# Kernel tuning notes

Hardware: AMD Instinct MI355X
Metric: run time of the kernel (lower is better)

## Reference

```python
import jax, jax.numpy as jnp
import numpy as np

HIDDEN = 1024
B, S = 64, 512
EPS = 1e-10


def setup_inputs() -> dict:
    key = jax.random.key(0)
    k1, k2, k3, k4, k5 = jax.random.split(key, 5)
    encoder_outputs = jax.random.normal(k1, (B, S, HIDDEN), dtype=jnp.float32)
    decoder_hidden = jax.random.normal(k2, (B, HIDDEN), dtype=jnp.float32)
    inp_mask = (jax.random.uniform(k3, (S, B)) > 0.2).astype(jnp.float32)
    # W_h: Linear(2H -> H, bias=False); torch stores weight as (out, in)
    W_h = jax.random.normal(k4, (HIDDEN, 2 * HIDDEN), dtype=jnp.float32) / np.sqrt(2 * HIDDEN)
    stdv = 1.0 / np.sqrt(HIDDEN)
    v = jax.random.normal(k5, (HIDDEN,), dtype=jnp.float32) * stdv
    return {"encoder_outputs": encoder_outputs, "decoder_hidden": decoder_hidden,
            "inp_mask": inp_mask, "W_h": W_h, "v": v}


def reference(encoder_outputs, decoder_hidden, inp_mask, W_h, v):
    # encoder_outputs: [B, S, H]; decoder_hidden: [B, H]; inp_mask: [S, B]
    seq_len = encoder_outputs.shape[1]
    # H = decoder_hidden broadcast over seq: [B, S, H] (avoid explicit repeat)
    Hrep = jnp.broadcast_to(decoder_hidden[:, None, :], encoder_outputs.shape)
    cat = jnp.concatenate([Hrep, encoder_outputs], axis=2)          # [B, S, 2H]
    energy = jnp.tanh(jnp.einsum('bsk,hk->bsh', cat, W_h))          # [B, S, H]
    scores = jnp.einsum('bsh,h->bs', energy, v)                     # [B, S]
    # NOTE: original applies softmax over dim=0 (the batch dim) — faithful here
    a = jax.nn.softmax(scores, axis=0) * inp_mask.T                 # [B, S]
    a = a / (jnp.sum(a, axis=1, keepdims=True) + EPS)
    context = jnp.einsum('bs,bsh->bh', a, encoder_outputs)[:, None, :]  # [B, 1, H]
    return a[:, None, :], context
```

## Files before the change

### kernel.cpp

```cpp
#include <hip/hip_runtime.h>

#define B_ 64
#define S_ 512
#define H_ 1024
#define M_ (B_*S_)

typedef unsigned int u32;
typedef unsigned short u16;
typedef __attribute__((ext_vector_type(8))) short bf16x8;
typedef __attribute__((ext_vector_type(4))) float f32x4;

__device__ __forceinline__ u16 f2bf(float f) {
  u32 u = __builtin_bit_cast(u32, f);
  u += 0x7fffu + ((u >> 16) & 1u);
  return (u16)(u >> 16);
}
__device__ __forceinline__ u32 pk2(float a, float b) {
  return (u32)f2bf(a) | ((u32)f2bf(b) << 16);
}
__device__ __forceinline__ float tanh_fast(float x) {
  x = fminf(fmaxf(x, -20.f), 20.f);
  float e = __expf(2.f * x);
  return (e - 1.f) / (e + 1.f);
}
__device__ __forceinline__ void gload_lds16(const u16* g, u16* l) {
  __builtin_amdgcn_global_load_lds(
      (const __attribute__((address_space(1))) u32*)g,
      (__attribute__((address_space(3))) u32*)l, 16, 0, 0);
}

__global__ void conv_w2(const float* __restrict__ Wh, u16* __restrict__ W2bf) {
  int idx = blockIdx.x * 256 + threadIdx.x;
  int n = idx >> 8;
  int k = (idx & 255) * 4;
  float4 x = *(const float4*)(Wh + (size_t)n * 2048 + 1024 + k);
  uint2 p; p.x = pk2(x.x, x.y); p.y = pk2(x.z, x.w);
  *(uint2*)(W2bf + (size_t)n * 1024 + k) = p;
}

__global__ void part1_kernel(const float* __restrict__ dh,
                             const float* __restrict__ Wh,
                             float* __restrict__ part1) {
  __shared__ float whs[16][132];
  __shared__ float dhs[64][132];
  int t = threadIdx.x;
  int h0 = blockIdx.x * 16;
  int k0 = blockIdx.y * 128;
#pragma unroll
  for (int i = 0; i < 2; ++i) {
    int idx = t + 256 * i;
    int r = idx >> 5, c4 = idx & 31;
    float4 x = *(const float4*)(Wh + (size_t)(h0 + r) * 2048 + k0 + c4 * 4);
    *(float4*)&whs[r][c4 * 4] = x;
  }
#pragma unroll
  for (int i = 0; i < 8; ++i) {
    int idx = t + 256 * i;
    int r = idx >> 5, c4 = idx & 31;
    float4 x = *(const float4*)(dh + (size_t)r * 1024 + k0 + c4 * 4);
    *(float4*)&dhs[r][c4 * 4] = x;
  }
  __syncthreads();
  int b = t >> 2, hg = t & 3;
  float acc[4] = {0.f, 0.f, 0.f, 0.f};
#pragma unroll 4
  for (int k = 0; k < 128; ++k) {
    float d = dhs[b][k];
#pragma unroll
    for (int j = 0; j < 4; ++j) acc[j] += whs[hg * 4 + j][k] * d;
  }
#pragma unroll
  for (int j = 0; j < 4; ++j)
    atomicAdd(&part1[b * 1024 + h0 + hg * 4 + j], acc[j]);
}

__global__ __launch_bounds__(256, 2) void gemm_scores(
    const float* __restrict__ enc, const u16* __restrict__ W2bf,
    const float* __restrict__ part1, const float* __restrict__ v,
    float* __restrict__ scores) {
  __shared__ __align__(16) u16 As[2][128 * 64];
  __shared__ __align__(16) u16 Bs[2][128 * 64];
  __shared__ float sc_lds[128];
  const int tid = threadIdx.x;
  const int lane = tid & 63, wid = tid >> 6;
  const int wr = wid >> 1, wc = wid & 1;
  const int l15 = lane & 15, lhi = lane >> 4;
  const int n0 = blockIdx.x * 128;
  const int r0 = blockIdx.y * 128;
  const int bb = r0 >> 9;

  f32x4 acc[4][4] = {};

  const int brow8 = lane >> 3;
  const int bks = ((lane & 7) ^ brow8) * 8;

  {
#pragma unroll
    for (int c = 0; c < 4; ++c) {
      const u16* src = W2bf + (size_t)(n0 + c * 32 + wid * 8 + brow8) * 1024 + bks;
      gload_lds16(src, &Bs[0][c * 2048 + wid * 512]);
    }
#pragma unroll
    for (int i = 0; i < 4; ++i) {
      int f = 2 * tid + 512 * i;
      int arow = f >> 4, c4 = f & 15;
      const float4* srcA = (const float4*)(enc + (size_t)(r0 + arow) * 1024 + c4 * 4);
      float4 x = srcA[0], y = srcA[1];
      uint4 p; p.x = pk2(x.x, x.y); p.y = pk2(x.z, x.w);
      p.z = pk2(y.x, y.y); p.w = pk2(y.z, y.w);
      *(uint4*)&As[0][arow * 64 + ((c4 * 4) ^ ((arow & 7) << 3))] = p;
    }
    __syncthreads();
  }

  int p = 0;
  for (int t = 0; t < 16; ++t) {
    float4 xa[4], ya[4];
    if (t < 15) {
      const int kn = (t + 1) * 64;
#pragma unroll
      for (int c = 0; c < 4; ++c) {
        const u16* src =
            W2bf + (size_t)(n0 + c * 32 + wid * 8 + brow8) * 1024 + kn + bks;
        gload_lds16(src, &Bs[p ^ 1][c * 2048 + wid * 512]);
      }
#pragma unroll
      for (int i = 0; i < 4; ++i) {
        int f = 2 * tid + 512 * i;
        int arow = f >> 4, c4 = f & 15;
        const float4* srcA =
            (const float4*)(enc + (size_t)(r0 + arow) * 1024 + kn + c4 * 4);
        xa[i] = srcA[0]; ya[i] = srcA[1];
      }
    }
#pragma unroll
    for (int kk = 0; kk < 2; ++kk) {
      bf16x8 af[4], bfr[4];
#pragma unroll
      for (int i = 0; i < 4; ++i) {
        int ar = wr * 64 + i * 16 + l15;
        af[i] = *(const bf16x8*)&As[p][ar * 64 + ((kk * 32 + lhi * 8) ^ ((ar & 7) << 3))];
      }
#pragma unroll
      for (int j = 0; j < 4; ++j) {
        int br = wc * 64 + j * 16 + l15;
        bfr[j] = *(const bf16x8*)&Bs[p][br * 64 + ((kk * 32 + lhi * 8) ^ ((br & 7) << 3))];
      }
#pragma unroll
      for (int i = 0; i < 4; ++i)
#pragma unroll
        for (int j = 0; j < 4; ++j)
          acc[i][j] = __builtin_amdgcn_mfma_f32_16x16x32_bf16(
              af[i], bfr[j], acc[i][j], 0, 0, 0);
    }
    if (t < 15) {
#pragma unroll
      for (int i = 0; i < 4; ++i) {
        int f = 2 * tid + 512 * i;
        int arow = f >> 4, c4 = f & 15;
        uint4 pw;
        pw.x = pk2(xa[i].x, xa[i].y); pw.y = pk2(xa[i].z, xa[i].w);
        pw.z = pk2(ya[i].x, ya[i].y); pw.w = pk2(ya[i].z, ya[i].w);
        *(uint4*)&As[p ^ 1][arow * 64 + ((c4 * 4) ^ ((arow & 7) << 3))] = pw;
      }
      __syncthreads();
      p ^= 1;
    }
  }

  if (tid < 128) sc_lds[tid] = 0.f;
  __syncthreads();
  float ps[4][4] = {};
#pragma unroll
  for (int j = 0; j < 4; ++j) {
    int col = n0 + wc * 64 + j * 16 + l15;
    float pv = part1[bb * 1024 + col];
    float vv = v[col];
#pragma unroll
    for (int i = 0; i < 4; ++i)
#pragma unroll
      for (int q = 0; q < 4; ++q)
        ps[i][q] += tanh_fast(acc[i][j][q] + pv) * vv;
  }
#pragma unroll
  for (int i = 0; i < 4; ++i)
#pragma unroll
    for (int q = 0; q < 4; ++q)
      atomicAdd(&sc_lds[wr * 64 + i * 16 + lhi * 4 + q], ps[i][q]);
  __syncthreads();
  if (tid < 128) atomicAdd(&scores[r0 + tid], sc_lds[tid]);
}

__global__ void softmax_col(const float* __restrict__ scores,
                            const float* __restrict__ mask,
                            float* __restrict__ a_raw) {
  int s = blockIdx.x;
  int b = threadIdx.x;
  float x = scores[b * 512 + s];
  float m = x;
  for (int o = 32; o; o >>= 1) m = fmaxf(m, __shfl_xor(m, o));
  float e = __expf(x - m);
  float sum = e;
  for (int o = 32; o; o >>= 1) sum += __shfl_xor(sum, o);
  a_raw[b * 512 + s] = (e / sum) * mask[s * 64 + b];
}

__global__ void norm_rows(const float* __restrict__ a_raw,
                          float* __restrict__ out_a) {
  __shared__ float wsum[4];
  int b = blockIdx.x, t = threadIdx.x;
  float va = a_raw[b * 512 + t];
  float vb = a_raw[b * 512 + 256 + t];
  float sum = va + vb;
  for (int o = 32; o; o >>= 1) sum += __shfl_xor(sum, o);
  if ((t & 63) == 0) wsum[t >> 6] = sum;
  __syncthreads();
  float tot = wsum[0] + wsum[1] + wsum[2] + wsum[3];
  float inv = 1.f / (tot + 1e-10f);
  out_a[b * 512 + t] = va * inv;
  out_a[b * 512 + 256 + t] = vb * inv;
}

__global__ void context_kernel(const float* __restrict__ a,
                               const float* __restrict__ enc,
                               float* __restrict__ ctx) {
  int b = blockIdx.x, hc = blockIdx.y, sc = blockIdx.z, t = threadIdx.x;
  int h = hc * 256 + t;
  const float* ep = enc + (size_t)b * 512 * 1024 + (size_t)sc * 64 * 1024 + h;
  const float* ap = a + b * 512 + sc * 64;
  float acc = 0.f;
#pragma unroll 8
  for (int s = 0; s < 64; ++s) acc += ap[s] * ep[(size_t)s * 1024];
  atomicAdd(&ctx[b * 1024 + h], acc);
}

extern "C" void kernel_launch(void* const* d_in, const int* in_sizes, int n_in,
                              void* d_out, int out_size, void* d_ws,
                              size_t ws_size, hipStream_t stream) {
  const float* enc  = (const float*)d_in[0];
  const float* dh   = (const float*)d_in[1];
  const float* mask = (const float*)d_in[2];
  const float* Wh   = (const float*)d_in[3];
  const float* v    = (const float*)d_in[4];
  float* out_a   = (float*)d_out;
  float* out_ctx = out_a + M_;

  char* ws = (char*)d_ws;
  u16*   W2bf   = (u16*)ws;
  float* part1  = (float*)(ws + (2u << 20));
  float* scores = (float*)(ws + (2u << 20) + (256u << 10));
  float* a_raw  = (float*)(ws + (2u << 20) + (384u << 10));

  hipMemsetAsync(scores, 0, M_ * sizeof(float), stream);
  hipMemsetAsync(part1, 0, B_ * H_ * sizeof(float), stream);
  hipMemsetAsync(out_ctx, 0, B_ * H_ * sizeof(float), stream);
  conv_w2<<<1024, 256, 0, stream>>>(Wh, W2bf);
  part1_kernel<<<dim3(64, 8), 256, 0, stream>>>(dh, Wh, part1);
  gemm_scores<<<dim3(8, 256), 256, 0, stream>>>(enc, W2bf, part1, v, scores);
  softmax_col<<<512, 64, 0, stream>>>(scores, mask, a_raw);
  norm_rows<<<64, 256, 0, stream>>>(a_raw, out_a);
  context_kernel<<<dim3(64, 4, 8), 256, 0, stream>>>(out_a, enc, out_ctx);
}
```

Measured before the change: 446.0 us.

## Pre-convert encoder to bf16, swizzle GEMM tiles, and drop atomics and memsets

When the workspace is large enough, the encoder outputs are converted to bf16 once in a separate kernel. The GEMM then streams both operands straight into LDS with global_load_lds, instead of loading fp32 and converting in registers every time. GEMM blocks are remapped so groups of row tiles share column tiles for better L2 reuse, and per-column-tile partial scores go to separate buffers rather than global atomics. The part1, softmax and context kernels are restructured to accumulate without atomics or memsets. The trade-off is an extra full pass writing a 64MB bf16 copy of the encoder, and a context kernel with fewer blocks and longer serial loops.

```diff
diff --git a/kernel.cpp b/kernel.cpp
--- a/kernel.cpp
+++ b/kernel.cpp
@@ -27,6 +27,26 @@
   __builtin_amdgcn_global_load_lds(
       (const __attribute__((address_space(1))) u32*)g,
       (__attribute__((address_space(3))) u32*)l, 16, 0, 0);
+}
+
+__device__ __forceinline__ void decode_bid(int bid, int& r0, int& n0) {
+  int nt = (bid >> 3) & 7;
+  int rp = ((bid >> 6) << 3) | (bid & 7);
+  r0 = rp * 128; n0 = nt * 128;
+}
+
+__global__ void conv_enc(const float* __restrict__ e, u16* __restrict__ o) {
+  int g0 = blockIdx.x * 2048 + threadIdx.x;
+#pragma unroll
+  for (int j = 0; j < 8; ++j) {
+    int g = g0 + j * 256;
+    const float4* s = (const float4*)(e + (size_t)g * 8);
+    float4 x = s[0], y = s[1];
+    uint4 p;
+    p.x = pk2(x.x, x.y); p.y = pk2(x.z, x.w);
+    p.z = pk2(y.x, y.y); p.w = pk2(y.z, y.w);
+    *(uint4*)(o + (size_t)g * 8) = p;
+  }
 }
 
 __global__ void conv_w2(const float* __restrict__ Wh, u16* __restrict__ W2bf) {
@@ -45,39 +65,39 @@
   __shared__ float dhs[64][132];
   int t = threadIdx.x;
   int h0 = blockIdx.x * 16;
-  int k0 = blockIdx.y * 128;
-#pragma unroll
-  for (int i = 0; i < 2; ++i) {
-    int idx = t + 256 * i;
-    int r = idx >> 5, c4 = idx & 31;
-    float4 x = *(const float4*)(Wh + (size_t)(h0 + r) * 2048 + k0 + c4 * 4);
-    *(float4*)&whs[r][c4 * 4] = x;
-  }
-#pragma unroll
-  for (int i = 0; i < 8; ++i) {
-    int idx = t + 256 * i;
-    int r = idx >> 5, c4 = idx & 31;
-    float4 x = *(const float4*)(dh + (size_t)r * 1024 + k0 + c4 * 4);
-    *(float4*)&dhs[r][c4 * 4] = x;
-  }
-  __syncthreads();
   int b = t >> 2, hg = t & 3;
   float acc[4] = {0.f, 0.f, 0.f, 0.f};
+  for (int kc = 0; kc < 8; ++kc) {
+    int k0 = kc * 128;
+    __syncthreads();
+#pragma unroll
+    for (int i = 0; i < 2; ++i) {
+      int idx = t + 256 * i; int r = idx >> 5, c4 = idx & 31;
+      *(float4*)&whs[r][c4 * 4] =
+          *(const float4*)(Wh + (size_t)(h0 + r) * 2048 + k0 + c4 * 4);
+    }
+#pragma unroll
+    for (int i = 0; i < 8; ++i) {
+      int idx = t + 256 * i; int r = idx >> 5, c4 = idx & 31;
+      *(float4*)&dhs[r][c4 * 4] =
+          *(const float4*)(dh + (size_t)r * 1024 + k0 + c4 * 4);
+    }
+    __syncthreads();
 #pragma unroll 4
-  for (int k = 0; k < 128; ++k) {
-    float d = dhs[b][k];
-#pragma unroll
-    for (int j = 0; j < 4; ++j) acc[j] += whs[hg * 4 + j][k] * d;
-  }
-#pragma unroll
-  for (int j = 0; j < 4; ++j)
-    atomicAdd(&part1[b * 1024 + h0 + hg * 4 + j], acc[j]);
-}
-
-__global__ __launch_bounds__(256, 2) void gemm_scores(
-    const float* __restrict__ enc, const u16* __restrict__ W2bf,
+    for (int k = 0; k < 128; ++k) {
+      float d = dhs[b][k];
+#pragma unroll
+      for (int j = 0; j < 4; ++j) acc[j] += whs[hg * 4 + j][k] * d;
+    }
+  }
+#pragma unroll
+  for (int j = 0; j < 4; ++j) part1[b * 1024 + h0 + hg * 4 + j] = acc[j];
+}
+
+__global__ __launch_bounds__(256, 2) void gemm_scores_bf(
+    const u16* __restrict__ Abf, const u16* __restrict__ W2bf,
     const float* __restrict__ part1, const float* __restrict__ v,
-    float* __restrict__ scores) {
+    float* __restrict__ scores_part) {
   __shared__ __align__(16) u16 As[2][128 * 64];
   __shared__ __align__(16) u16 Bs[2][128 * 64];
   __shared__ float sc_lds[128];
@@ -85,45 +105,129 @@
   const int lane = tid & 63, wid = tid >> 6;
   const int wr = wid >> 1, wc = wid & 1;
   const int l15 = lane & 15, lhi = lane >> 4;
-  const int n0 = blockIdx.x * 128;
-  const int r0 = blockIdx.y * 128;
+  int r0, n0; decode_bid(blockIdx.x, r0, n0);
+  const int nt = n0 >> 7;
   const int bb = r0 >> 9;
-
   f32x4 acc[4][4] = {};
 
+  int sofs[4];
+#pragma unroll
+  for (int i = 0; i < 4; ++i) {
+    int idx = i * 256 + tid;
+    int row = idx >> 3, g = idx & 7;
+    sofs[i] = row * 1024 + ((g ^ (row & 7)) << 3);
+  }
+
+#define STAGE_T(pbuf, kk0)                                                   \
+  do {                                                                       \
+    _Pragma("unroll") for (int i_ = 0; i_ < 4; ++i_)                         \
+        gload_lds16(Abf + (size_t)r0 * 1024 + (kk0) + sofs[i_],              \
+                    &As[pbuf][i_ * 2048 + wid * 512]);                       \
+    _Pragma("unroll") for (int i_ = 0; i_ < 4; ++i_)                         \
+        gload_lds16(W2bf + (size_t)n0 * 1024 + (kk0) + sofs[i_],             \
+                    &Bs[pbuf][i_ * 2048 + wid * 512]);                       \
+  } while (0)
+
+  STAGE_T(0, 0);
+  __syncthreads();
+  int p = 0;
+  for (int t = 0; t < 16; ++t) {
+    if (t < 15) STAGE_T(p ^ 1, (t + 1) * 64);
+#pragma unroll
+    for (int kk = 0; kk < 2; ++kk) {
+      bf16x8 af[4], bfr[4];
+#pragma unroll
+      for (int i = 0; i < 4; ++i) {
+        int ar = wr * 64 + i * 16 + l15;
+        af[i] = *(const bf16x8*)
+            &As[p][ar * 64 + (((kk * 4 + lhi) ^ (ar & 7)) << 3)];
+      }
+#pragma unroll
+      for (int j = 0; j < 4; ++j) {
+        int br = wc * 64 + j * 16 + l15;
+        bfr[j] = *(const bf16x8*)
+            &Bs[p][br * 64 + (((kk * 4 + lhi) ^ (br & 7)) << 3)];
+      }
+#pragma unroll
+      for (int i = 0; i < 4; ++i)
+#pragma unroll
+        for (int j = 0; j < 4; ++j)
+          acc[i][j] = __builtin_amdgcn_mfma_f32_16x16x32_bf16(
+              af[i], bfr[j], acc[i][j], 0, 0, 0);
+    }
+    __syncthreads();
+    p ^= 1;
+  }
+#undef STAGE_T
+
+  if (tid < 128) sc_lds[tid] = 0.f;
+  __syncthreads();
+  float ps[4][4] = {};
+#pragma unroll
+  for (int j = 0; j < 4; ++j) {
+    int col = n0 + wc * 64 + j * 16 + l15;
+    float pv = part1[bb * 1024 + col];
+    float vv = v[col];
+#pragma unroll
+    for (int i = 0; i < 4; ++i)
+#pragma unroll
+      for (int q = 0; q < 4; ++q)
+        ps[i][q] += tanh_fast(acc[i][j][q] + pv) * vv;
+  }
+#pragma unroll
+  for (int i = 0; i < 4; ++i)
+#pragma unroll
+    for (int q = 0; q < 4; ++q)
+      atomicAdd(&sc_lds[wr * 64 + i * 16 + lhi * 4 + q], ps[i][q]);
+  __syncthreads();
+  if (tid < 128) scores_part[nt * M_ + r0 + tid] = sc_lds[tid];
+}
+
+__global__ __launch_bounds__(256, 2) void gemm_scores_inline(
+    const float* __restrict__ enc, const u16* __restrict__ W2bf,
+    const float* __restrict__ part1, const float* __restrict__ v,
+    float* __restrict__ scores_part) {
+  __shared__ __align__(16) u16 As[2][128 * 64];
+  __shared__ __align__(16) u16 Bs[2][128 * 64];
+  __shared__ float sc_lds[128];
+  const int tid = threadIdx.x;
+  const int lane = tid & 63, wid = tid >> 6;
+  const int wr = wid >> 1, wc = wid & 1;
+  const int l15 = lane & 15, lhi = lane >> 4;
+  int r0, n0; decode_bid(blockIdx.x, r0, n0);
+  const int nt = n0 >> 7;
+  const int bb = r0 >> 9;
+  f32x4 acc[4][4] = {};
   const int brow8 = lane >> 3;
   const int bks = ((lane & 7) ^ brow8) * 8;
-
   {
 #pragma unroll
-    for (int c = 0; c < 4; ++c) {
-      const u16* src = W2bf + (size_t)(n0 + c * 32 + wid * 8 + brow8) * 1024 + bks;
-      gload_lds16(src, &Bs[0][c * 2048 + wid * 512]);
-    }
+    for (int c = 0; c < 4; ++c)
+      gload_lds16(W2bf + (size_t)(n0 + c * 32 + wid * 8 + brow8) * 1024 + bks,
+                  &Bs[0][c * 2048 + wid * 512]);
 #pragma unroll
     for (int i = 0; i < 4; ++i) {
       int f = 2 * tid + 512 * i;
       int arow = f >> 4, c4 = f & 15;
-      const float4* srcA = (const float4*)(enc + (size_t)(r0 + arow) * 1024 + c4 * 4);
+      const float4* srcA =
+          (const float4*)(enc + (size_t)(r0 + arow) * 1024 + c4 * 4);
       float4 x = srcA[0], y = srcA[1];
-      uint4 p; p.x = pk2(x.x, x.y); p.y = pk2(x.z, x.w);
-      p.z = pk2(y.x, y.y); p.w = pk2(y.z, y.w);
-      *(uint4*)&As[0][arow * 64 + ((c4 * 4) ^ ((arow & 7) << 3))] = p;
+      uint4 pw; pw.x = pk2(x.x, x.y); pw.y = pk2(x.z, x.w);
+      pw.z = pk2(y.x, y.y); pw.w = pk2(y.z, y.w);
+      *(uint4*)&As[0][arow * 64 + ((c4 * 4) ^ ((arow & 7) << 3))] = pw;
     }
     __syncthreads();
   }
-
   int p = 0;
   for (int t = 0; t < 16; ++t) {
     float4 xa[4], ya[4];
     if (t < 15) {
       const int kn = (t + 1) * 64;
 #pragma unroll
-      for (int c = 0; c < 4; ++c) {
-        const u16* src =
-            W2bf + (size_t)(n0 + c * 32 + wid * 8 + brow8) * 1024 + kn + bks;
-        gload_lds16(src, &Bs[p ^ 1][c * 2048 + wid * 512]);
-      }
+      for (int c = 0; c < 4; ++c)
+        gload_lds16(
+            W2bf + (size_t)(n0 + c * 32 + wid * 8 + brow8) * 1024 + kn + bks,
+            &Bs[p ^ 1][c * 2048 + wid * 512]);
 #pragma unroll
       for (int i = 0; i < 4; ++i) {
         int f = 2 * tid + 512 * i;
@@ -139,12 +243,14 @@
 #pragma unroll
       for (int i = 0; i < 4; ++i) {
         int ar = wr * 64 + i * 16 + l15;
-        af[i] = *(const bf16x8*)&As[p][ar * 64 + ((kk * 32 + lhi * 8) ^ ((ar & 7) << 3))];
+        af[i] = *(const bf16x8*)
+            &As[p][ar * 64 + ((kk * 32 + lhi * 8) ^ ((ar & 7) << 3))];
       }
 #pragma unroll
       for (int j = 0; j < 4; ++j) {
         int br = wc * 64 + j * 16 + l15;
-        bfr[j] = *(const bf16x8*)&Bs[p][br * 64 + ((kk * 32 + lhi * 8) ^ ((br & 7) << 3))];
+        bfr[j] = *(const bf16x8*)
+            &Bs[p][br * 64 + ((kk * 32 + lhi * 8) ^ ((br & 7) << 3))];
       }
 #pragma unroll
       for (int i = 0; i < 4; ++i)
@@ -167,7 +273,6 @@
       p ^= 1;
     }
   }
-
   if (tid < 128) sc_lds[tid] = 0.f;
   __syncthreads();
   float ps[4][4] = {};
@@ -188,15 +293,17 @@
     for (int q = 0; q < 4; ++q)
       atomicAdd(&sc_lds[wr * 64 + i * 16 + lhi * 4 + q], ps[i][q]);
   __syncthreads();
-  if (tid < 128) atomicAdd(&scores[r0 + tid], sc_lds[tid]);
-}
-
-__global__ void softmax_col(const float* __restrict__ scores,
+  if (tid < 128) scores_part[nt * M_ + r0 + tid] = sc_lds[tid];
+}
+
+__global__ void softmax_col(const float* __restrict__ sp,
                             const float* __restrict__ mask,
                             float* __restrict__ a_raw) {
-  int s = blockIdx.x;
-  int b = threadIdx.x;
-  float x = scores[b * 512 + s];
+  int s = blockIdx.x * 4 + (threadIdx.x >> 6);
+  int b = threadIdx.x & 63;
+  float x = 0.f;
+#pragma unroll
+  for (int n = 0; n < 8; ++n) x += sp[n * M_ + b * 512 + s];
   float m = x;
   for (int o = 32; o; o >>= 1) m = fmaxf(m, __shfl_xor(m, o));
   float e = __expf(x - m);
@@ -224,14 +331,18 @@
 __global__ void context_kernel(const float* __restrict__ a,
                                const float* __restrict__ enc,
                                float* __restrict__ ctx) {
-  int b = blockIdx.x, hc = blockIdx.y, sc = blockIdx.z, t = threadIdx.x;
-  int h = hc * 256 + t;
-  const float* ep = enc + (size_t)b * 512 * 1024 + (size_t)sc * 64 * 1024 + h;
-  const float* ap = a + b * 512 + sc * 64;
+  __shared__ float red[128];
+  int b = blockIdx.x, hc = blockIdx.y, t = threadIdx.x;
+  int h = hc * 128 + (t & 127);
+  int sh = t >> 7;
+  const float* ep = enc + (size_t)b * 524288 + (size_t)sh * 262144 + h;
+  const float* ap = a + b * 512 + sh * 256;
   float acc = 0.f;
 #pragma unroll 8
-  for (int s = 0; s < 64; ++s) acc += ap[s] * ep[(size_t)s * 1024];
-  atomicAdd(&ctx[b * 1024 + h], acc);
+  for (int s = 0; s < 256; ++s) acc += ap[s] * ep[(size_t)s * 1024];
+  if (sh) red[t & 127] = acc;
+  __syncthreads();
+  if (!sh) ctx[b * 1024 + h] = acc + red[t];
 }
 
 extern "C" void kernel_launch(void* const* d_in, const int* in_sizes, int n_in,
@@ -246,18 +357,32 @@
   float* out_ctx = out_a + M_;
 
   char* ws = (char*)d_ws;
-  u16*   W2bf   = (u16*)ws;
-  float* part1  = (float*)(ws + (2u << 20));
-  float* scores = (float*)(ws + (2u << 20) + (256u << 10));
-  float* a_raw  = (float*)(ws + (2u << 20) + (384u << 10));
-
-  hipMemsetAsync(scores, 0, M_ * sizeof(float), stream);
-  hipMemsetAsync(part1, 0, B_ * H_ * sizeof(float), stream);
-  hipMemsetAsync(out_ctx, 0, B_ * H_ * sizeof(float), stream);
+  const size_t SZ_ENC = (size_t)M_ * H_ * 2;
+  u16*   W2bf; u16* encbf = nullptr;
+  float *part1, *sp, *a_raw;
+  bool big = ws_size >= SZ_ENC + (4u << 20);
+  if (big) {
+    encbf = (u16*)ws;
+    W2bf  = (u16*)(ws + SZ_ENC);
+    part1 = (float*)(ws + SZ_ENC + (2u << 20));
+    sp    = (float*)(ws + SZ_ENC + (2u << 20) + (256u << 10));
+    a_raw = (float*)(ws + SZ_ENC + (2u << 20) + (256u << 10) + (1u << 20));
+  } else {
+    W2bf  = (u16*)ws;
+    part1 = (float*)(ws + (2u << 20));
+    sp    = (float*)(ws + (2u << 20) + (256u << 10));
+    a_raw = (float*)(ws + (2u << 20) + (256u << 10) + (1u << 20));
+  }
+
   conv_w2<<<1024, 256, 0, stream>>>(Wh, W2bf);
-  part1_kernel<<<dim3(64, 8), 256, 0, stream>>>(dh, Wh, part1);
-  gemm_scores<<<dim3(8, 256), 256, 0, stream>>>(enc, W2bf, part1, v, scores);
-  softmax_col<<<512, 64, 0, stream>>>(scores, mask, a_raw);
+  part1_kernel<<<64, 256, 0, stream>>>(dh, Wh, part1);
+  if (big) {
+    conv_enc<<<2048, 256, 0, stream>>>(enc, encbf);
+    gemm_scores_bf<<<2048, 256, 0, stream>>>(encbf, W2bf, part1, v, sp);
+  } else {
+    gemm_scores_inline<<<2048, 256, 0, stream>>>(enc, W2bf, part1, v, sp);
+  }
+  softmax_col<<<128, 256, 0, stream>>>(sp, mask, a_raw);
   norm_rows<<<64, 256, 0, stream>>>(a_raw, out_a);
-  context_kernel<<<dim3(64, 4, 8), 256, 0, stream>>>(out_a, enc, out_ctx);
-}
+  context_kernel<<<dim3(64, 8), 256, 0, stream>>>(out_a, enc, out_ctx);
+}
```

Result: faster. 436.0 us (-2.2%).
